# Kernel tuning notes

Hardware: AMD Instinct MI355X
Metric: run time of the kernel (lower is better)

The kernel has to match this reference:

```python
import jax, jax.numpy as jnp
import numpy as np
import itertools

LN_EPS = 1e-3  # keras LayerNormalization default epsilon

def _pair_indices(field_num):
    pairs = np.array(list(itertools.combinations(range(field_num), 2)), dtype=np.int32)
    return pairs[:, 0], pairs[:, 1]

def setup_inputs() -> dict:
    key = jax.random.key(0)
    ks = jax.random.split(key, 3)
    B, F, E, P, D = 2048, 40, 32, 780, 16
    x = jax.random.normal(ks[0], (B, F, E), dtype=jnp.float32)
    # glorot-normal-ish scaling for the bilinear pair weights
    W = jax.random.normal(ks[1], (P, E, E), dtype=jnp.float32) * (2.0 / (E + E)) ** 0.5
    dense_w = jax.random.normal(ks[2], (P, D), dtype=jnp.float32) * (2.0 / (P + D)) ** 0.5
    dense_b = jnp.zeros((D,), dtype=jnp.float32)
    gamma = jnp.ones((D,), dtype=jnp.float32)
    beta = jnp.zeros((D,), dtype=jnp.float32)
    return {"x": x, "W": W, "dense_w": dense_w, "dense_b": dense_b,
            "gamma": gamma, "beta": beta}

def reference(x, W, dense_w, dense_b, gamma, beta):
    F = x.shape[1]
    idx_i, idx_j = _pair_indices(F)           # static pair lists, P = C(F,2)
    xi = x[:, idx_i, :]                        # [B, P, E]
    xj = x[:, idx_j, :]                        # [B, P, E]
    # (x_i @ W_p) . x_j per pair, fused: p[b,p] = sum_ef xi[b,p,e] W[p,e,f] xj[b,p,f]
    t = jnp.einsum('bpe,pef->bpf', xi, W)      # [B, P, E]
    p = jnp.einsum('bpf,bpf->bp', t, xj)       # [B, P]
    # reducing layer: Dense(output_dim) + LayerNorm (no activation)
    h = p @ dense_w + dense_b                  # [B, D]
    mu = jnp.mean(h, axis=-1, keepdims=True)
    var = jnp.mean(jnp.square(h - mu), axis=-1, keepdims=True)
    out = (h - mu) * jax.lax.rsqrt(var + LN_EPS) * gamma + beta
    return out
```

## Files before the change

### kernel.cpp

```cpp
#include <hip/hip_runtime.h>
#include <hip/hip_bf16.h>

typedef __attribute__((ext_vector_type(8))) short bf16x8;
typedef __attribute__((ext_vector_type(4))) float f32x4;
typedef __attribute__((ext_vector_type(4))) unsigned short u16x4;

#define B_NUM 2048
#define F_NUM 40
#define E_DIM 32
#define P_NUM 780
#define D_DIM 16
#define PC_N  65
#define PC_SZ 12
#define LN_EPS 1e-3f

#define XB_OFF  0
#define XB_BYTES (F_NUM * 4 * B_NUM * 8 * 2)
#define HP_OFF  XB_BYTES

static __device__ __forceinline__ unsigned short f2b(float f) {
  unsigned u = __builtin_bit_cast(unsigned, f);
  u += 0x7fffu + ((u >> 16) & 1u);
  return (unsigned short)(u >> 16);
}
static __device__ __forceinline__ short f2bs(float f) { return (short)f2b(f); }
static __device__ __forceinline__ short fcvt(float f) {
  return (short)__bfloat16_as_ushort(__float2bfloat16(f));
}
static __device__ __forceinline__ float b2f(unsigned short u) {
  return __builtin_bit_cast(float, (unsigned)u << 16);
}

__global__ __launch_bounds__(256) void xpack_kernel(
    const float* __restrict__ x, short* __restrict__ xbp) {
  const int u  = blockIdx.x * 256 + threadIdx.x;
  const int b  = u & (B_NUM - 1);
  const int fp = u >> 11;
  const int f  = fp >> 1;
  const float* src = x + ((size_t)b * F_NUM + f) * E_DIM + (fp & 1) * 16;
  const float4 v0 = *reinterpret_cast<const float4*>(src);
  const float4 v1 = *reinterpret_cast<const float4*>(src + 4);
  const float4 v2 = *reinterpret_cast<const float4*>(src + 8);
  const float4 v3 = *reinterpret_cast<const float4*>(src + 12);
  const int plane = f * 4 + (fp & 1) * 2;
  bf16x8 o0, o1;
  o0[0] = f2bs(v0.x); o0[1] = f2bs(v0.y); o0[2] = f2bs(v0.z); o0[3] = f2bs(v0.w);
  o0[4] = f2bs(v1.x); o0[5] = f2bs(v1.y); o0[6] = f2bs(v1.z); o0[7] = f2bs(v1.w);
  o1[0] = f2bs(v2.x); o1[1] = f2bs(v2.y); o1[2] = f2bs(v2.z); o1[3] = f2bs(v2.w);
  o1[4] = f2bs(v3.x); o1[5] = f2bs(v3.y); o1[6] = f2bs(v3.z); o1[7] = f2bs(v3.w);
  *reinterpret_cast<bf16x8*>(xbp + ((size_t)plane * B_NUM + b) * 8)       = o0;
  *reinterpret_cast<bf16x8*>(xbp + ((size_t)(plane + 1) * B_NUM + b) * 8) = o1;
}

__global__ __launch_bounds__(256, 2) void fused_bilinear_dense_kernel(
    const float* __restrict__ W, const float* __restrict__ dw,
    const short* __restrict__ xbp, unsigned short* __restrict__ hpart) {
  __shared__ unsigned short wraw[PC_SZ * 1024];
  __shared__ __align__(16) unsigned short afrag[PC_SZ * 2 * 512];
  const int tid  = threadIdx.x;
  const int lane = tid & 63, wv = tid >> 6;
  const int lhi = lane >> 4, llo = lane & 15;
  const int bb = blockIdx.x * 256 + wv * 64;
  const int pc = blockIdx.y;
  const int p0 = pc * PC_SZ;

  {
    const float* Wsrc = W + (size_t)p0 * 1024;
#pragma unroll
    for (int it = 0; it < PC_SZ; ++it) {
      const int L = it * 1024 + tid * 4;
      float4 v = *reinterpret_cast<const float4*>(Wsrc + L);
      u16x4 o;
      o[0] = f2b(v.x); o[1] = f2b(v.y); o[2] = f2b(v.z); o[3] = f2b(v.w);
      *reinterpret_cast<u16x4*>(&wraw[L]) = o;
    }
  }
  __syncthreads();

#pragma unroll
  for (int s = 0; s < 3; ++s) {
    const int pl = wv * 3 + s;
#pragma unroll
    for (int frag = 0; frag < 2; ++frag) {
      const int fo = (llo >> 2) * 8 + frag * 4 + (llo & 3);
      bf16x8 v;
#pragma unroll
      for (int t = 0; t < 8; ++t)
        v[t] = (short)wraw[pl * 1024 + (lhi * 8 + t) * E_DIM + fo];
      *reinterpret_cast<bf16x8*>(&afrag[(pl * 2 + frag) * 512 + lane * 8]) = v;
    }
  }
  __syncthreads();

  int off[4];
#pragma unroll
  for (int nt = 0; nt < 4; ++nt)
    off[nt] = (lhi * B_NUM + bb + nt * 16 + llo) * 8;
#define XB8(f, o) (*reinterpret_cast<const bf16x8*>(xbp + (size_t)(f) * 65536 + (o)))

  int ii[PC_SZ], jj[PC_SZ];
  {
    int i = 0;
    while ((i + 1) * (79 - (i + 1)) / 2 <= p0) ++i;
    ii[0] = i; jj[0] = i + 1 + (p0 - i * (79 - i) / 2);
  }
#pragma unroll
  for (int k = 1; k < PC_SZ; ++k) {
    int in_ = ii[k - 1], jn = jj[k - 1] + 1;
    if (jn == F_NUM) { ++in_; jn = in_ + 1; }
    ii[k] = in_; jj[k] = jn;
  }

  bf16x8 bf[4];
#pragma unroll
  for (int nt = 0; nt < 4; ++nt) bf[nt] = XB8(ii[0], off[nt]);

  bf16x8 sxj[2][4];
  float sdwf[2];
#pragma unroll
  for (int s = 0; s < 2; ++s) {
#pragma unroll
    for (int nt = 0; nt < 4; ++nt) sxj[s][nt] = XB8(jj[s], off[nt]);
    sdwf[s] = dw[(p0 + s) * D_DIM + llo];
  }

  f32x4 acc[4];
#pragma unroll
  for (int nt = 0; nt < 4; ++nt) acc[nt] = {0.f, 0.f, 0.f, 0.f};
  const f32x4 z = {0.f, 0.f, 0.f, 0.f};

#pragma unroll
  for (int k = 0; k < PC_SZ; ++k) {
    const int s = k & 1;
    const bf16x8 xj0 = sxj[s][0], xj1 = sxj[s][1];
    const bf16x8 xj2 = sxj[s][2], xj3 = sxj[s][3];
    const float dwf = sdwf[s];
    if (k + 2 < PC_SZ) {
#pragma unroll
      for (int nt = 0; nt < 4; ++nt) sxj[s][nt] = XB8(jj[k + 2], off[nt]);
      sdwf[s] = dw[(p0 + k + 2) * D_DIM + llo];
    }

    const bf16x8 a0 = *reinterpret_cast<const bf16x8*>(&afrag[(k * 2 + 0) * 512 + lane * 8]);
    const bf16x8 a1 = *reinterpret_cast<const bf16x8*>(&afrag[(k * 2 + 1) * 512 + lane * 8]);

    __builtin_amdgcn_s_setprio(1);
    f32x4 c0[4], c1[4];
#pragma unroll
    for (int nt = 0; nt < 4; ++nt) {
      c0[nt] = __builtin_amdgcn_mfma_f32_16x16x32_bf16(a0, bf[nt], z, 0, 0, 0);
      c1[nt] = __builtin_amdgcn_mfma_f32_16x16x32_bf16(a1, bf[nt], z, 0, 0, 0);
    }

    const short dwb = fcvt(dwf);
    bf16x8 a2;
#pragma unroll
    for (int t = 0; t < 8; ++t) a2[t] = dwb;

    const bf16x8 xjl[4] = {xj0, xj1, xj2, xj3};
#pragma unroll
    for (int nt = 0; nt < 4; ++nt) {
      bf16x8 u;
#pragma unroll
      for (int t = 0; t < 4; ++t) {
        u[t]     = fcvt(c0[nt][t] * b2f((unsigned short)xjl[nt][t]));
        u[t + 4] = fcvt(c1[nt][t] * b2f((unsigned short)xjl[nt][t + 4]));
      }
      acc[nt] = __builtin_amdgcn_mfma_f32_16x16x32_bf16(a2, u, acc[nt], 0, 0, 0);
    }
    __builtin_amdgcn_s_setprio(0);

    if (k + 1 < PC_SZ && ii[k + 1] != ii[k]) {
#pragma unroll
      for (int nt = 0; nt < 4; ++nt) bf[nt] = XB8(ii[k + 1], off[nt]);
    }
  }
#undef XB8

  unsigned short* hp = hpart + (size_t)pc * B_NUM * D_DIM;
#pragma unroll
  for (int nt = 0; nt < 4; ++nt) {
    u16x4 o;
    o[0] = f2b(acc[nt][0]); o[1] = f2b(acc[nt][1]);
    o[2] = f2b(acc[nt][2]); o[3] = f2b(acc[nt][3]);
    *reinterpret_cast<u16x4*>(
        hp + (size_t)(bb + nt * 16 + llo) * D_DIM + lhi * 4) = o;
  }
}

__global__ __launch_bounds__(256) void reduce_ln_kernel(
    const unsigned short* __restrict__ hpart, const float* __restrict__ bias,
    const float* __restrict__ gamma, const float* __restrict__ beta,
    float* __restrict__ out) {
  const int g  = blockIdx.x * 256 + threadIdx.x;
  const int b  = g >> 3;
  const int d2 = g & 7;
  const uint* hp = reinterpret_cast<const uint*>(hpart) + (size_t)b * 8 + d2;

  float h0 = bias[2 * d2], h1 = bias[2 * d2 + 1];
#pragma unroll 13
  for (int pc = 0; pc < PC_N; ++pc) {
    const uint v = hp[(size_t)pc * B_NUM * 8];
    h0 += b2f((unsigned short)v);
    h1 += b2f((unsigned short)(v >> 16));
  }

  float sum = h0 + h1;
  sum += __shfl_xor(sum, 1); sum += __shfl_xor(sum, 2); sum += __shfl_xor(sum, 4);
  const float mu = sum * (1.f / D_DIM);
  const float dv0 = h0 - mu, dv1 = h1 - mu;
  float v = dv0 * dv0 + dv1 * dv1;
  v += __shfl_xor(v, 1); v += __shfl_xor(v, 2); v += __shfl_xor(v, 4);
  const float rs = rsqrtf(v * (1.f / D_DIM) + LN_EPS);

  float2 o;
  o.x = dv0 * rs * gamma[2 * d2]     + beta[2 * d2];
  o.y = dv1 * rs * gamma[2 * d2 + 1] + beta[2 * d2 + 1];
  *reinterpret_cast<float2*>(out + (size_t)b * D_DIM + 2 * d2) = o;
}

extern "C" void kernel_launch(void* const* d_in, const int* in_sizes, int n_in,
                              void* d_out, int out_size, void* d_ws, size_t ws_size,
                              hipStream_t stream) {
  const float* x     = (const float*)d_in[0];
  const float* W     = (const float*)d_in[1];
  const float* dw    = (const float*)d_in[2];
  const float* db    = (const float*)d_in[3];
  const float* gamma = (const float*)d_in[4];
  const float* beta  = (const float*)d_in[5];
  float* out = (float*)d_out;

  short*          xbp   = (short*)((char*)d_ws + XB_OFF);
  unsigned short* hpart = (unsigned short*)((char*)d_ws + HP_OFF);

  xpack_kernel<<<640, 256, 0, stream>>>(x, xbp);

  dim3 gA(B_NUM / 256, PC_N);
  fused_bilinear_dense_kernel<<<gA, 256, 0, stream>>>(W, dw, xbp, hpart);

  reduce_ln_kernel<<<B_NUM * 8 / 256, 256, 0, stream>>>(hpart, db, gamma, beta, out);
}
```

Before: 29.58 us.

## Tile pairs into 4x4 field blocks to reuse x rows across pairs

The work is now split into 4x4 blocks of field pairs (45 off-diagonal plus 10 diagonal tiles) instead of 12 consecutive pairs per block. Each wave loads only 2 xi rows and 4 xj rows from global memory and reuses them across up to 8 pairs. The batch tile shrinks to 128, with two waves splitting the pairs and combining their partial sums through shared memory before the store. The aim is less redundant global traffic for x. In exchange, diagonal tiles leave some waves idle, the grid grows, and shared memory use rises.

New measurement: 41.77 us. 1.41x slower.

```diff
diff --git a/kernel.cpp b/kernel.cpp
--- a/kernel.cpp
+++ b/kernel.cpp
@@ -10,8 +10,8 @@
 #define E_DIM 32
 #define P_NUM 780
 #define D_DIM 16
-#define PC_N  65
-#define PC_SZ 12
+#define NT_FULL 45
+#define NT_ALL  55
 #define LN_EPS 1e-3f
 
 #define XB_OFF  0
@@ -55,38 +55,52 @@
 __global__ __launch_bounds__(256, 2) void fused_bilinear_dense_kernel(
     const float* __restrict__ W, const float* __restrict__ dw,
     const short* __restrict__ xbp, unsigned short* __restrict__ hpart) {
-  __shared__ unsigned short wraw[PC_SZ * 1024];
-  __shared__ __align__(16) unsigned short afrag[PC_SZ * 2 * 512];
+  __shared__ unsigned short wraw[16 * 1024];
+  __shared__ __align__(16) unsigned short afrag[16 * 2 * 512];
+  __shared__ float redbuf[4 * 64 * 16];
+
   const int tid  = threadIdx.x;
   const int lane = tid & 63, wv = tid >> 6;
   const int lhi = lane >> 4, llo = lane & 15;
-  const int bb = blockIdx.x * 256 + wv * 64;
-  const int pc = blockIdx.y;
-  const int p0 = pc * PC_SZ;
-
-  {
-    const float* Wsrc = W + (size_t)p0 * 1024;
-#pragma unroll
-    for (int it = 0; it < PC_SZ; ++it) {
-      const int L = it * 1024 + tid * 4;
-      float4 v = *reinterpret_cast<const float4*>(Wsrc + L);
+  const int ph = wv >> 1;
+  const int pv = wv & 1;
+  const int bb = blockIdx.x * 128 + ph * 64;
+  const int t  = blockIdx.y;
+
+  int I, J;
+  if (t < NT_FULL) {
+    I = 0;
+    while (9 * (I + 1) - (I + 1) * I / 2 <= t) ++I;
+    J = I + 1 + (t - (9 * I - I * (I - 1) / 2));
+  } else {
+    I = t - NT_FULL; J = I;
+  }
+  const bool diag = (I == J);
+
+#pragma unroll
+  for (int idx = 0; idx < 16; ++idx) {
+    const int i = 4 * I + (idx >> 2), j = 4 * J + (idx & 3);
+    if (j > i) {
+      const int p = i * (79 - i) / 2 + (j - i - 1);
+      const float4 v = *reinterpret_cast<const float4*>(
+          W + (size_t)p * 1024 + tid * 4);
       u16x4 o;
       o[0] = f2b(v.x); o[1] = f2b(v.y); o[2] = f2b(v.z); o[3] = f2b(v.w);
-      *reinterpret_cast<u16x4*>(&wraw[L]) = o;
+      *reinterpret_cast<u16x4*>(&wraw[idx * 1024 + tid * 4]) = o;
     }
   }
   __syncthreads();
 
 #pragma unroll
-  for (int s = 0; s < 3; ++s) {
-    const int pl = wv * 3 + s;
+  for (int q = 0; q < 4; ++q) {
+    const int pl = wv * 4 + q;
 #pragma unroll
     for (int frag = 0; frag < 2; ++frag) {
       const int fo = (llo >> 2) * 8 + frag * 4 + (llo & 3);
       bf16x8 v;
 #pragma unroll
-      for (int t = 0; t < 8; ++t)
-        v[t] = (short)wraw[pl * 1024 + (lhi * 8 + t) * E_DIM + fo];
+      for (int tt = 0; tt < 8; ++tt)
+        v[tt] = (short)wraw[pl * 1024 + (lhi * 8 + tt) * E_DIM + fo];
       *reinterpret_cast<bf16x8*>(&afrag[(pl * 2 + frag) * 512 + lane * 8]) = v;
     }
   }
@@ -98,31 +112,20 @@
     off[nt] = (lhi * B_NUM + bb + nt * 16 + llo) * 8;
 #define XB8(f, o) (*reinterpret_cast<const bf16x8*>(xbp + (size_t)(f) * 65536 + (o)))
 
-  int ii[PC_SZ], jj[PC_SZ];
-  {
-    int i = 0;
-    while ((i + 1) * (79 - (i + 1)) / 2 <= p0) ++i;
-    ii[0] = i; jj[0] = i + 1 + (p0 - i * (79 - i) / 2);
-  }
-#pragma unroll
-  for (int k = 1; k < PC_SZ; ++k) {
-    int in_ = ii[k - 1], jn = jj[k - 1] + 1;
-    if (jn == F_NUM) { ++in_; jn = in_ + 1; }
-    ii[k] = in_; jj[k] = jn;
-  }
-
-  bf16x8 bf[4];
-#pragma unroll
-  for (int nt = 0; nt < 4; ++nt) bf[nt] = XB8(ii[0], off[nt]);
-
-  bf16x8 sxj[2][4];
-  float sdwf[2];
+  bf16x8 bxi[2][4], bxj[4][4];
 #pragma unroll
   for (int s = 0; s < 2; ++s) {
-#pragma unroll
-    for (int nt = 0; nt < 4; ++nt) sxj[s][nt] = XB8(jj[s], off[nt]);
-    sdwf[s] = dw[(p0 + s) * D_DIM + llo];
-  }
+    const int irow = 4 * I + pv * 2 + s;
+#pragma unroll
+    for (int nt = 0; nt < 4; ++nt) bxi[s][nt] = XB8(irow, off[nt]);
+  }
+#pragma unroll
+  for (int b = 0; b < 4; ++b) {
+    const int jrow = 4 * J + b;
+#pragma unroll
+    for (int nt = 0; nt < 4; ++nt) bxj[b][nt] = XB8(jrow, off[nt]);
+  }
+#undef XB8
 
   f32x4 acc[4];
 #pragma unroll
@@ -130,61 +133,66 @@
   const f32x4 z = {0.f, 0.f, 0.f, 0.f};
 
 #pragma unroll
-  for (int k = 0; k < PC_SZ; ++k) {
-    const int s = k & 1;
-    const bf16x8 xj0 = sxj[s][0], xj1 = sxj[s][1];
-    const bf16x8 xj2 = sxj[s][2], xj3 = sxj[s][3];
-    const float dwf = sdwf[s];
-    if (k + 2 < PC_SZ) {
-#pragma unroll
-      for (int nt = 0; nt < 4; ++nt) sxj[s][nt] = XB8(jj[k + 2], off[nt]);
-      sdwf[s] = dw[(p0 + k + 2) * D_DIM + llo];
-    }
-
-    const bf16x8 a0 = *reinterpret_cast<const bf16x8*>(&afrag[(k * 2 + 0) * 512 + lane * 8]);
-    const bf16x8 a1 = *reinterpret_cast<const bf16x8*>(&afrag[(k * 2 + 1) * 512 + lane * 8]);
-
-    __builtin_amdgcn_s_setprio(1);
-    f32x4 c0[4], c1[4];
-#pragma unroll
-    for (int nt = 0; nt < 4; ++nt) {
-      c0[nt] = __builtin_amdgcn_mfma_f32_16x16x32_bf16(a0, bf[nt], z, 0, 0, 0);
-      c1[nt] = __builtin_amdgcn_mfma_f32_16x16x32_bf16(a1, bf[nt], z, 0, 0, 0);
-    }
-
-    const short dwb = fcvt(dwf);
-    bf16x8 a2;
-#pragma unroll
-    for (int t = 0; t < 8; ++t) a2[t] = dwb;
-
-    const bf16x8 xjl[4] = {xj0, xj1, xj2, xj3};
-#pragma unroll
-    for (int nt = 0; nt < 4; ++nt) {
-      bf16x8 u;
-#pragma unroll
-      for (int t = 0; t < 4; ++t) {
-        u[t]     = fcvt(c0[nt][t] * b2f((unsigned short)xjl[nt][t]));
-        u[t + 4] = fcvt(c1[nt][t] * b2f((unsigned short)xjl[nt][t + 4]));
+  for (int s = 0; s < 2; ++s) {
+    const int a = pv * 2 + s;
+    const int i = 4 * I + a;
+#pragma unroll
+    for (int b = 0; b < 4; ++b) {
+      const int j = 4 * J + b;
+      if (diag && j <= i) continue;
+      const int p   = i * (79 - i) / 2 + (j - i - 1);
+      const int idx = a * 4 + b;
+
+      const bf16x8 a0 = *reinterpret_cast<const bf16x8*>(
+          &afrag[(idx * 2 + 0) * 512 + lane * 8]);
+      const bf16x8 a1 = *reinterpret_cast<const bf16x8*>(
+          &afrag[(idx * 2 + 1) * 512 + lane * 8]);
+      const short dwb = fcvt(dw[p * D_DIM + llo]);
+
+      __builtin_amdgcn_s_setprio(1);
+      f32x4 c0[4], c1[4];
+#pragma unroll
+      for (int nt = 0; nt < 4; ++nt) {
+        c0[nt] = __builtin_amdgcn_mfma_f32_16x16x32_bf16(a0, bxi[s][nt], z, 0, 0, 0);
+        c1[nt] = __builtin_amdgcn_mfma_f32_16x16x32_bf16(a1, bxi[s][nt], z, 0, 0, 0);
       }
-      acc[nt] = __builtin_amdgcn_mfma_f32_16x16x32_bf16(a2, u, acc[nt], 0, 0, 0);
-    }
-    __builtin_amdgcn_s_setprio(0);
-
-    if (k + 1 < PC_SZ && ii[k + 1] != ii[k]) {
-#pragma unroll
-      for (int nt = 0; nt < 4; ++nt) bf[nt] = XB8(ii[k + 1], off[nt]);
-    }
-  }
-#undef XB8
-
-  unsigned short* hp = hpart + (size_t)pc * B_NUM * D_DIM;
-#pragma unroll
-  for (int nt = 0; nt < 4; ++nt) {
-    u16x4 o;
-    o[0] = f2b(acc[nt][0]); o[1] = f2b(acc[nt][1]);
-    o[2] = f2b(acc[nt][2]); o[3] = f2b(acc[nt][3]);
-    *reinterpret_cast<u16x4*>(
-        hp + (size_t)(bb + nt * 16 + llo) * D_DIM + lhi * 4) = o;
+      bf16x8 a2;
+#pragma unroll
+      for (int tt = 0; tt < 8; ++tt) a2[tt] = dwb;
+#pragma unroll
+      for (int nt = 0; nt < 4; ++nt) {
+        bf16x8 u;
+#pragma unroll
+        for (int tt = 0; tt < 4; ++tt) {
+          u[tt]     = fcvt(c0[nt][tt] * b2f((unsigned short)bxj[b][nt][tt]));
+          u[tt + 4] = fcvt(c1[nt][tt] * b2f((unsigned short)bxj[b][nt][tt + 4]));
+        }
+        acc[nt] = __builtin_amdgcn_mfma_f32_16x16x32_bf16(a2, u, acc[nt], 0, 0, 0);
+      }
+      __builtin_amdgcn_s_setprio(0);
+    }
+  }
+
+#pragma unroll
+  for (int nt = 0; nt < 4; ++nt)
+#pragma unroll
+    for (int r = 0; r < 4; ++r)
+      redbuf[wv * 1024 + (nt * 16 + llo) * 16 + lhi * 4 + r] = acc[nt][r];
+  __syncthreads();
+
+  {
+    const int v0  = tid * 8;
+    const int ph2 = v0 >> 10;
+    const int q   = v0 & 1023;
+    bf16x8 ov;
+#pragma unroll
+    for (int e = 0; e < 8; ++e) {
+      const float val = redbuf[(ph2 * 2 + 0) * 1024 + q + e] +
+                        redbuf[(ph2 * 2 + 1) * 1024 + q + e];
+      ov[e] = f2bs(val);
+    }
+    *reinterpret_cast<bf16x8*>(
+        hpart + (size_t)t * (B_NUM * D_DIM) + blockIdx.x * 2048 + ph2 * 1024 + q) = ov;
   }
 }
 
@@ -198,8 +206,8 @@
   const uint* hp = reinterpret_cast<const uint*>(hpart) + (size_t)b * 8 + d2;
 
   float h0 = bias[2 * d2], h1 = bias[2 * d2 + 1];
-#pragma unroll 13
-  for (int pc = 0; pc < PC_N; ++pc) {
+#pragma unroll 11
+  for (int pc = 0; pc < NT_ALL; ++pc) {
     const uint v = hp[(size_t)pc * B_NUM * 8];
     h0 += b2f((unsigned short)v);
     h1 += b2f((unsigned short)(v >> 16));
@@ -235,7 +243,7 @@
 
   xpack_kernel<<<640, 256, 0, stream>>>(x, xbp);
 
-  dim3 gA(B_NUM / 256, PC_N);
+  dim3 gA(B_NUM / 128, NT_ALL);
   fused_bilinear_dense_kernel<<<gA, 256, 0, stream>>>(W, dw, xbp, hpart);
 
   reduce_ln_kernel<<<B_NUM * 8 / 256, 256, 0, stream>>>(hpart, db, gamma, beta, out);
```
